# Kernel tuning notes

Hardware: AMD Instinct MI355X
Metric: run time of the kernel (lower is better)

The kernel has to match this reference:

```python
import jax, jax.numpy as jnp
import numpy as np

B, S, E, H = 4, 1024, 1024, 16
HD = E // H
MAX_SEQ = 5000


def setup_inputs() -> dict:
    key = jax.random.key(0)
    ks = jax.random.split(key, 10)
    def lin(kw, kb):
        w = jax.random.normal(kw, (E, E), dtype=jnp.float32) * (1.0 / np.sqrt(E))
        b = jax.random.normal(kb, (E,), dtype=jnp.float32) * 0.01
        return w, b
    wq, bq = lin(ks[0], ks[1])
    wk, bk = lin(ks[2], ks[3])
    wv, bv = lin(ks[4], ks[5])
    wo, bo = lin(ks[6], ks[7])
    rpe_table = jax.random.normal(ks[8], (H, 2 * MAX_SEQ - 1, HD), dtype=jnp.float32) * 0.02
    x = jax.random.normal(ks[9], (B, S, E), dtype=jnp.float32)
    return {"x": x, "wq": wq, "bq": bq, "wk": wk, "bk": bk,
            "wv": wv, "bv": bv, "wo": wo, "bo": bo, "rpe_table": rpe_table}


def reference(x, wq, bq, wk, bk, wv, bv, wo, bo, rpe_table):
    b, s, e = x.shape
    scale = 1.0 / np.sqrt(HD)
    # projections (torch Linear: y = x @ W^T + b), reshape to (b, h, s, hd)
    q = (x @ wq.T + bq).reshape(b, s, H, HD).transpose(0, 2, 1, 3)
    k = (x @ wk.T + bk).reshape(b, s, H, HD).transpose(0, 2, 1, 3)
    v = (x @ wv.T + bv).reshape(b, s, H, HD).transpose(0, 2, 1, 3)
    scores = jnp.einsum('bhqd,bhkd->bhqk', q, k) * scale
    # RPE: rpe[h, q, k, d] = table[h, q - k + s - 1, d]; factor the einsum:
    # rel[b,h,q,r] = sum_d q[b,h,q,d] * table[h,r,d], then gather r = q - k + s - 1
    table = rpe_table[:, : 2 * s - 1]               # (H, 2s-1, HD)
    rel = jnp.einsum('bhqd,hrd->bhqr', q, table)    # (b, H, s, 2s-1)
    idx = jnp.arange(s)[:, None] - jnp.arange(s)[None, :] + (s - 1)  # (s, s)
    rpe_scores = jnp.take_along_axis(
        rel, jnp.broadcast_to(idx[None, None], (b, H, s, s)), axis=-1)
    attn = jax.nn.softmax(scores + rpe_scores, axis=-1)
    ctx = jnp.einsum('bhqk,bhkd->bhqd', attn, v)
    ctx = ctx.transpose(0, 2, 1, 3).reshape(b, s, e)
    return ctx @ wo.T + bo
```

## Files before the change

kernel.cpp:

```cpp
#include <hip/hip_runtime.h>
#include <hip/hip_bf16.h>
#include <stdint.h>

typedef __attribute__((ext_vector_type(8))) short s8v;
typedef __attribute__((ext_vector_type(4))) float f32x4;
typedef __attribute__((ext_vector_type(16))) float f32x16;

union V16 { uint4 u4; unsigned int u[4]; s8v s; };

__device__ inline s8v u4_to_s8(uint4 v) { V16 c; c.u4 = v; return c.s; }
__device__ inline s8v words_to_s8(unsigned int a, unsigned int b, unsigned int c, unsigned int d) {
  V16 t; t.u[0] = a; t.u[1] = b; t.u[2] = c; t.u[3] = d; return t.s;
}
__device__ inline unsigned short f2b(float f) {
  __hip_bfloat16 h = __float2bfloat16(f);
  unsigned short u; __builtin_memcpy(&u, &h, 2); return u;
}
__device__ inline unsigned int pack2(float lo, float hi) {
  return ((unsigned int)f2b(hi) << 16) | (unsigned int)f2b(lo);
}
__device__ inline unsigned int cvtpk(float lo, float hi) {
  unsigned int r; asm("v_cvt_pk_bf16_f32 %0, %1, %2" : "=v"(r) : "v"(lo), "v"(hi)); return r;
}
__device__ inline float exp2_fast(float x) {
#if __has_builtin(__builtin_amdgcn_exp2f)
  return __builtin_amdgcn_exp2f(x);
#else
  float y; asm("v_exp_f32 %0, %1" : "=v"(y) : "v"(x)); return y;
#endif
}
__device__ inline void gld16(const void* g, void* lds) {
  __builtin_amdgcn_global_load_lds((const __attribute__((address_space(1))) void*)g,
                                   (__attribute__((address_space(3))) void*)lds, 16, 0, 0);
}

#define LOG2E 1.4426950408889634f

__global__ void cvt_fused_kernel(const float* __restrict__ x, const float* __restrict__ wq,
                                 const float* __restrict__ wk, const float* __restrict__ wv,
                                 const float* __restrict__ wo, const float* __restrict__ tb,
                                 __hip_bfloat16* __restrict__ XB, __hip_bfloat16* __restrict__ WQKV,
                                 __hip_bfloat16* __restrict__ WOb, __hip_bfloat16* __restrict__ TBL) {
  const int bid = blockIdx.x;
  if (bid < 4096) {
    size_t i = ((size_t)bid * 256 + threadIdx.x) * 8;
    const float* src; __hip_bfloat16* dst; size_t off;
    if (i < 4194304)      { src = x;  dst = XB;             off = i; }
    else if (i < 5242880) { src = wq; dst = WQKV;           off = i - 4194304; }
    else if (i < 6291456) { src = wk; dst = WQKV + 1048576; off = i - 5242880; }
    else if (i < 7340032) { src = wv; dst = WQKV + 2097152; off = i - 6291456; }
    else                  { src = wo; dst = WOb;            off = i - 7340032; }
    const float4* s4 = (const float4*)(src + off);
    float4 a = s4[0], b = s4[1];
    uint4 o;
    o.x = pack2(a.x, a.y); o.y = pack2(a.z, a.w);
    o.z = pack2(b.x, b.y); o.w = pack2(b.z, b.w);
    *(uint4*)(dst + off) = o;
  } else {
    size_t i = ((size_t)(bid - 4096) * 256 + threadIdx.x) * 8;
    int h = (int)(i >> 17);
    int rem = (int)(i & 131071);
    int r = rem >> 6, c = rem & 63;
    uint4 o;
    if (r < 2047) {
      const float4* s4 = (const float4*)(tb + ((size_t)h * 9999 + r) * 64 + c);
      float4 a = s4[0], b = s4[1];
      o.x = pack2(a.x * LOG2E, a.y * LOG2E); o.y = pack2(a.z * LOG2E, a.w * LOG2E);
      o.z = pack2(b.x * LOG2E, b.y * LOG2E); o.w = pack2(b.z * LOG2E, b.w * LOG2E);
    } else { o.x = 0u; o.y = 0u; o.z = 0u; o.w = 0u; }
    *(uint4*)(TBL + i) = o;
  }
}

__global__ __launch_bounds__(256, 3) void gemm_qkv(
    const __hip_bfloat16* __restrict__ A,
    const __hip_bfloat16* __restrict__ Bt,
    const float* __restrict__ bq, const float* __restrict__ bk, const float* __restrict__ bv,
    __hip_bfloat16* __restrict__ QB, __hip_bfloat16* __restrict__ KB,
    __hip_bfloat16* __restrict__ VTB) {
  __shared__ __align__(16) char smem[32768];
  char* As = smem;
  char* Bs = smem + 16384;
  const int tid = threadIdx.x;
  const int w = tid >> 6, l = tid & 63;
  const int wr = w >> 1, wc = w & 1;
  const int lr = l & 15, lg = l >> 4;
  const int m0 = blockIdx.y * 128, n0 = blockIdx.x * 128;

  f32x4 acc[4][4] = {};

  for (int kt = 0; kt < 16; ++kt) {
    __syncthreads();
    #pragma unroll
    for (int i = 0; i < 4; ++i) {
      const int off = i * 4096 + w * 1024;
      const int loff = off + l * 16;
      const int row = loff >> 7;
      const int cb = loff & 127;
      const int sc = cb ^ ((row & 7) << 4);
      gld16((const char*)A  + (size_t)(m0 + row) * 2048 + kt * 128 + sc, As + off);
      gld16((const char*)Bt + (size_t)(n0 + row) * 2048 + kt * 128 + sc, Bs + off);
    }
    asm volatile("s_waitcnt vmcnt(0)" ::: "memory");
    __syncthreads();
    #pragma unroll
    for (int ks = 0; ks < 2; ++ks) {
      uint4 af[4], bf4[4];
      #pragma unroll
      for (int i = 0; i < 4; ++i) {
        const int ra = wr * 64 + i * 16 + lr;
        const int rb = wc * 64 + i * 16 + lr;
        const int cb = ks * 64 + lg * 16;
        af[i]  = *(const uint4*)(As + ra * 128 + (cb ^ ((ra & 7) << 4)));
        bf4[i] = *(const uint4*)(Bs + rb * 128 + (cb ^ ((rb & 7) << 4)));
      }
      #pragma unroll
      for (int i = 0; i < 4; ++i) {
        #pragma unroll
        for (int j = 0; j < 4; ++j)
          acc[i][j] = __builtin_amdgcn_mfma_f32_16x16x32_bf16(u4_to_s8(af[i]), u4_to_s8(bf4[j]), acc[i][j], 0, 0, 0);
      }
    }
  }

  const int mrow = m0 + wr * 64 + lg * 4;
  const int ncol = n0 + wc * 64 + lr;
  const int cls = blockIdx.x >> 3;

  if (cls < 2) {
    const float sc = cls ? 0.125f * LOG2E : 1.0f;
    const float* bias = cls ? bk : bq;
    __hip_bfloat16* op = cls ? KB : QB;
    #pragma unroll
    for (int j = 0; j < 4; ++j) {
      const int n = ncol - cls * 1024 + j * 16;
      const float bia = bias[n];
      const int hh = n >> 6, hd = n & 63;
      #pragma unroll
      for (int i = 0; i < 4; ++i) {
        #pragma unroll
        for (int r = 0; r < 4; ++r) {
          const int m = mrow + i * 16 + r;
          const int bb = m >> 10, ss = m & 1023;
          op[(((size_t)(bb * 16 + hh)) * 1024 + ss) * 64 + hd] = __float2bfloat16((acc[i][j][r] + bia) * sc);
        }
      }
    }
  } else {
    #pragma unroll
    for (int j = 0; j < 4; ++j) {
      const int f = ncol - 2048 + j * 16;
      const float bia = bv[f];
      const int fh = f >> 6, fd = f & 63;
      #pragma unroll
      for (int i = 0; i < 4; ++i) {
        const int m = mrow + i * 16;
        const int bb = m >> 10, ss = m & 1023;
        ushort4 qv;
        qv.x = f2b(acc[i][j][0] + bia); qv.y = f2b(acc[i][j][1] + bia);
        qv.z = f2b(acc[i][j][2] + bia); qv.w = f2b(acc[i][j][3] + bia);
        *(ushort4*)((char*)VTB + (((size_t)bb * 1048576 + (size_t)fh * 65536 + fd * 1024 + ss) * 2)) = qv;
      }
    }
  }
}

__global__ __launch_bounds__(256, 3) void gemm_out(
    const __hip_bfloat16* __restrict__ A,
    const __hip_bfloat16* __restrict__ Bt,
    const float* __restrict__ bo,
    float* __restrict__ out) {
  __shared__ __align__(16) char smem[32768];
  char* As = smem;
  char* Bs = smem + 16384;
  const int tid = threadIdx.x;
  const int w = tid >> 6, l = tid & 63;
  const int wr = w >> 1, wc = w & 1;
  const int lr = l & 15, lg = l >> 4;
  const int m0 = blockIdx.y * 128, n0 = blockIdx.x * 128;

  f32x4 acc[4][4] = {};

  for (int kt = 0; kt < 16; ++kt) {
    __syncthreads();
    #pragma unroll
    for (int i = 0; i < 4; ++i) {
      const int off = i * 4096 + w * 1024;
      const int loff = off + l * 16;
      const int row = loff >> 7;
      const int cb = loff & 127;
      const int sc = cb ^ ((row & 7) << 4);
      gld16((const char*)A  + (size_t)(m0 + row) * 2048 + kt * 128 + sc, As + off);
      gld16((const char*)Bt + (size_t)(n0 + row) * 2048 + kt * 128 + sc, Bs + off);
    }
    asm volatile("s_waitcnt vmcnt(0)" ::: "memory");
    __syncthreads();
    #pragma unroll
    for (int ks = 0; ks < 2; ++ks) {
      uint4 af[4], bf4[4];
      #pragma unroll
      for (int i = 0; i < 4; ++i) {
        const int ra = wr * 64 + i * 16 + lr;
        const int rb = wc * 64 + i * 16 + lr;
        const int cb = ks * 64 + lg * 16;
        af[i]  = *(const uint4*)(As + ra * 128 + (cb ^ ((ra & 7) << 4)));
        bf4[i] = *(const uint4*)(Bs + rb * 128 + (cb ^ ((rb & 7) << 4)));
      }
      #pragma unroll
      for (int i = 0; i < 4; ++i) {
        #pragma unroll
        for (int j = 0; j < 4; ++j)
          acc[i][j] = __builtin_amdgcn_mfma_f32_16x16x32_bf16(u4_to_s8(af[i]), u4_to_s8(bf4[j]), acc[i][j], 0, 0, 0);
      }
    }
  }

  const int mrow = m0 + wr * 64 + lg * 4;
  const int ncol = n0 + wc * 64 + lr;
  #pragma unroll
  for (int j = 0; j < 4; ++j) {
    const int n = ncol + j * 16;
    const float bia = bo[n];
    #pragma unroll
    for (int i = 0; i < 4; ++i) {
      #pragma unroll
      for (int r = 0; r < 4; ++r) {
        const int m = mrow + i * 16 + r;
        out[(size_t)m * 1024 + n] = acc[i][j][r] + bia;
      }
    }
  }
}

__global__ __launch_bounds__(256, 2) void attn_kernel(
    const __hip_bfloat16* __restrict__ Qg,
    const __hip_bfloat16* __restrict__ Kg,
    const __hip_bfloat16* __restrict__ VTg,
    const __hip_bfloat16* __restrict__ Tg,
    __hip_bfloat16* __restrict__ Cg) {
  __shared__ __align__(16) char smem[73984];
  char* Klds = smem;
  char* Vlds = smem + 8192;
  char* Tlds = smem + 16384;
  const int tid = threadIdx.x;
  const int w = tid >> 6, l = tid & 63;
  const int ql = l & 31, half = l >> 5;
  char* relw = smem + 40960 + w * 8192;
  char* dumpp = smem + 73728 + l * 4;

  const int bx = blockIdx.x;
  const int work = (bx & 7) * 64 + (bx >> 3);
  const int b = work & 3, hqt = work >> 2;
  const int h = hqt >> 3, qt = hqt & 7;
  const int qb = qt * 128;
  const int q0 = qb + 32 * w;

  const size_t bh = (size_t)(b * 16 + h);
  const char* Qb = (const char*)Qg + bh * 131072;
  const char* Kb = (const char*)Kg + bh * 131072;
  const char* Vb = (const char*)VTg + bh * 131072;
  const char* Tb = (const char*)Tg + (size_t)h * 262144;

  const int relsw = ql * 256 + ((ql & 15) << 4);
  const int u4 = (ql << 2) - (half << 4);
  const int qlh = ql - 4 * half;
  const int k0sw = ql * 128 + ((ql & 7) << 4);
  const int k1sw = (32 + ql) * 128 + ((ql & 7) << 4);

  auto stageK = [&](int k0n) {
    #pragma unroll
    for (int i = 0; i < 2; ++i) {
      const int off = i * 4096 + w * 1024;
      const int loff = off + l * 16;
      const int row = loff >> 7, cb = loff & 127;
      const int sc = cb ^ ((row & 7) << 4);
      gld16(Kb + (size_t)(k0n + row) * 128 + sc, Klds + off);
    }
  };
  auto stageV = [&](int k0n) {
    #pragma unroll
    for (int i = 0; i < 2; ++i) {
      const int off = i * 4096 + w * 1024;
      const int loff = off + l * 16;
      const int row = loff >> 7, cb = loff & 127;
      const int sc = cb ^ ((row & 7) << 4);
      gld16(Vb + (size_t)row * 2048 + (size_t)k0n * 2 + sc, Vlds + off);
    }
  };
  auto stageT = [&](int rbn) {
    const int slot = (int)(((unsigned)(rbn >> 6)) % 3u);
    char* dst = Tlds + slot * 8192;
    #pragma unroll
    for (int i = 0; i < 2; ++i) {
      const int off = i * 4096 + w * 1024;
      const int loff = off + l * 16;
      const int row = loff >> 7, cb = loff & 127;
      const int sc = cb ^ ((row & 7) << 4);
      gld16(Tb + (size_t)(rbn + row) * 128 + sc, dst + off);
    }
  };

  s8v qv[4];
  {
    const char* qrow = Qb + (size_t)(q0 + ql) * 128 + half * 16;
    #pragma unroll
    for (int ds = 0; ds < 4; ++ds) qv[ds] = u4_to_s8(*(const uint4*)(qrow + ds * 32));
  }

  f32x16 cacc0 = {}, cacc1 = {};
  float mL = -1.0e30f, lsum = 0.0f;

  int rbase = qb + 960;

  stageK(0);
  stageT(rbase); stageT(rbase + 64); stageT(rbase + 128);
  stageV(0);

  for (int kt = 0; kt < 16; ++kt, rbase -= 64) {
    if (kt == 0) { asm volatile("s_waitcnt vmcnt(8)" ::: "memory"); }
    else         { asm volatile("s_waitcnt vmcnt(4)" ::: "memory"); }
    __builtin_amdgcn_s_barrier();

    f32x16 p0 = {}, p1 = {};
    __builtin_amdgcn_s_setprio(1);
    #pragma unroll
    for (int ds = 0; ds < 4; ++ds) {
      const int cb = ds * 32 + half * 16;
      uint4 kf0 = *(const uint4*)(Klds + (k0sw ^ cb));
      uint4 kf1 = *(const uint4*)(Klds + (k1sw ^ cb));
      p0 = __builtin_amdgcn_mfma_f32_32x32x16_bf16(u4_to_s8(kf0), qv[ds], p0, 0, 0, 0);
      p1 = __builtin_amdgcn_mfma_f32_32x32x16_bf16(u4_to_s8(kf1), qv[ds], p1, 0, 0, 0);
    }
    __builtin_amdgcn_s_setprio(0);

    __builtin_amdgcn_s_barrier();
    stageK(((kt + 1) & 15) * 64);

    asm volatile("s_waitcnt vmcnt(4)" ::: "memory");
    __builtin_amdgcn_s_barrier();

    __builtin_amdgcn_s_setprio(1);
    #pragma unroll
    for (int t = 0; t < 3; ++t) {
      const int slot = (int)(((unsigned)(rbase >> 6) + (unsigned)((w + t) >> 1)) % 3u);
      const int rowin = ((w + t) & 1) * 32 + ql;
      const int tbsw = slot * 8192 + rowin * 128 + ((ql & 7) << 4);
      f32x16 racc = {};
      #pragma unroll
      for (int ds = 0; ds < 4; ++ds) {
        const int cb = ds * 32 + half * 16;
        uint4 tf = *(const uint4*)(Tlds + (tbsw ^ cb));
        racc = __builtin_amdgcn_mfma_f32_32x32x16_bf16(u4_to_s8(tf), qv[ds], racc, 0, 0, 0);
      }
      #pragma unroll
      for (int g = 0; g < 4; ++g) {
        #pragma unroll
        for (int j = 0; j < 4; ++j) {
          const int C4 = 4 * (63 - 32 * t - j - 8 * g);
          char* dst = relw + (relsw ^ ((u4 + C4) & 252));
          if (t == 2) dst = (j + 8 * g < qlh) ? dst : dumpp;
          *(float*)dst = racc[4 * g + j];
        }
      }
    }
    __builtin_amdgcn_s_setprio(0);

    __builtin_amdgcn_s_barrier();
    { int rbn = rbase - 64; if (rbn < 0) rbn = 0; stageT(rbn); }

    #pragma unroll
    for (int mp = 0; mp < 4; ++mp) {
      const int X0 = 32 * mp + 16 * half;
      f32x4 r0 = *(const f32x4*)(relw + (relsw ^ X0));
      f32x4 r1 = *(const f32x4*)(relw + (relsw ^ (X0 + 128)));
      #pragma unroll
      for (int j = 0; j < 4; ++j) {
        p0[4 * mp + j] += r0[j];
        p1[4 * mp + j] += r1[j];
      }
    }

    float mx[8];
    #pragma unroll
    for (int i = 0; i < 8; ++i)
      mx[i] = fmaxf(fmaxf(p0[2 * i], p0[2 * i + 1]), fmaxf(p1[2 * i], p1[2 * i + 1]));
    float pmax = fmaxf(fmaxf(fmaxf(mx[0], mx[1]), fmaxf(mx[2], mx[3])),
                       fmaxf(fmaxf(mx[4], mx[5]), fmaxf(mx[6], mx[7])));
    pmax = fmaxf(pmax, __shfl_xor(pmax, 32));
    if (!__all(pmax - mL <= 12.0f)) {
      const float mnew = fmaxf(mL, pmax);
      const float corr = exp2_fast(mL - mnew);
      mL = mnew;
      lsum *= corr;
      #pragma unroll
      for (int r = 0; r < 16; ++r) {
        const float cr = __shfl(corr, (r & 3) + 8 * (r >> 2) + 4 * half);
        cacc0[r] *= cr;
        cacc1[r] *= cr;
      }
    }
    #pragma unroll
    for (int r = 0; r < 16; ++r) {
      p0[r] = exp2_fast(p0[r] - mL);
      p1[r] = exp2_fast(p1[r] - mL);
    }
    float sm[8];
    #pragma unroll
    for (int i = 0; i < 8; ++i)
      sm[i] = (p0[2 * i] + p0[2 * i + 1]) + (p1[2 * i] + p1[2 * i + 1]);
    float psum = ((sm[0] + sm[1]) + (sm[2] + sm[3])) + ((sm[4] + sm[5]) + (sm[6] + sm[7]));
    psum += __shfl_xor(psum, 32);
    lsum += psum;

    unsigned int w0[8], w1[8];
    #pragma unroll
    for (int jw = 0; jw < 8; ++jw) {
      w0[jw] = cvtpk(p0[2 * jw], p0[2 * jw + 1]);
      w1[jw] = cvtpk(p1[2 * jw], p1[2 * jw + 1]);
    }
    unsigned int r0x[4], r1x[4];
    #pragma unroll
    for (int i = 0; i < 4; ++i) {
      const int jkeep = (i & 1) + 4 * (i >> 1);
      const int jsend = jkeep + 2;
      unsigned int v0 = half ? w0[jkeep] : w0[jsend];
      unsigned int v1 = half ? w1[jkeep] : w1[jsend];
      r0x[i] = (unsigned int)__shfl_xor((int)v0, 32);
      r1x[i] = (unsigned int)__shfl_xor((int)v1, 32);
    }

    asm volatile("s_waitcnt vmcnt(4)" ::: "memory");
    __builtin_amdgcn_s_barrier();

    __builtin_amdgcn_s_setprio(1);
    #pragma unroll
    for (int ks = 0; ks < 4; ++ks) {
      const int mm = ks & 1;
      unsigned int f0_, f1_, f2_, f3_;
      if (ks < 2) {
        f0_ = half ? r0x[2 * mm]     : w0[4 * mm];
        f1_ = half ? r0x[2 * mm + 1] : w0[4 * mm + 1];
        f2_ = half ? w0[4 * mm + 2]  : r0x[2 * mm];
        f3_ = half ? w0[4 * mm + 3]  : r0x[2 * mm + 1];
      } else {
        f0_ = half ? r1x[2 * mm]     : w1[4 * mm];
        f1_ = half ? r1x[2 * mm + 1] : w1[4 * mm + 1];
        f2_ = half ? w1[4 * mm + 2]  : r1x[2 * mm];
        f3_ = half ? w1[4 * mm + 3]  : r1x[2 * mm + 1];
      }
      s8v pf = words_to_s8(f0_, f1_, f2_, f3_);
      const int cb = ks * 32 + half * 16;
      uint4 vf0 = *(const uint4*)(Vlds + (k0sw ^ cb));
      uint4 vf1 = *(const uint4*)(Vlds + (k1sw ^ cb));
      cacc0 = __builtin_amdgcn_mfma_f32_32x32x16_bf16(pf, u4_to_s8(vf0), cacc0, 0, 0, 0);
      cacc1 = __builtin_amdgcn_mfma_f32_32x32x16_bf16(pf, u4_to_s8(vf1), cacc1, 0, 0, 0);
    }
    __builtin_amdgcn_s_setprio(0);

    __builtin_amdgcn_s_barrier();
    stageV(((kt + 1) & 15) * 64);
  }
  asm volatile("s_waitcnt vmcnt(0)" ::: "memory");

  #pragma unroll
  for (int r = 0; r < 16; ++r) {
    const int qr = (r & 3) + 8 * (r >> 2) + 4 * half;
    const float inv = 1.0f / __shfl(lsum, qr);
    const size_t row = (size_t)b * 1024 + q0 + qr;
    const size_t basei = row * 1024 + h * 64 + ql;
    Cg[basei]      = __float2bfloat16(cacc0[r] * inv);
    Cg[basei + 32] = __float2bfloat16(cacc1[r] * inv);
  }
}

extern "C" void kernel_launch(void* const* d_in, const int* in_sizes, int n_in,
                              void* d_out, int out_size, void* d_ws, size_t ws_size,
                              hipStream_t stream) {
  (void)in_sizes; (void)n_in; (void)out_size; (void)ws_size;
  const float* x  = (const float*)d_in[0];
  const float* wq = (const float*)d_in[1];
  const float* bq = (const float*)d_in[2];
  const float* wk = (const float*)d_in[3];
  const float* bk = (const float*)d_in[4];
  const float* wv = (const float*)d_in[5];
  const float* bv = (const float*)d_in[6];
  const float* wo = (const float*)d_in[7];
  const float* bo = (const float*)d_in[8];
  const float* tb = (const float*)d_in[9];

  char* ws = (char*)d_ws;
  __hip_bfloat16* XB   = (__hip_bfloat16*)(ws);
  __hip_bfloat16* WQKV = (__hip_bfloat16*)(ws + 8388608);
  __hip_bfloat16* WOb  = (__hip_bfloat16*)(ws + 14680064);
  __hip_bfloat16* TBL  = (__hip_bfloat16*)(ws + 16777216);
  __hip_bfloat16* QB   = (__hip_bfloat16*)(ws + 20971520);
  __hip_bfloat16* KB   = (__hip_bfloat16*)(ws + 29360128);
  __hip_bfloat16* VTB  = (__hip_bfloat16*)(ws + 37748736);
  __hip_bfloat16* CTX  = (__hip_bfloat16*)(ws + 46137344);

  cvt_fused_kernel<<<5120, 256, 0, stream>>>(x, wq, wk, wv, wo, tb, XB, WQKV, WOb, TBL);
  gemm_qkv<<<dim3(24, 32), 256, 0, stream>>>(XB, WQKV, bq, bk, bv, QB, KB, VTB);
  attn_kernel<<<512, 256, 0, stream>>>(QB, KB, VTB, TBL, CTX);
  gemm_out<<<dim3(8, 32), 256, 0, stream>>>(CTX, WOb, bo, (float*)d_out);
}
```

Baseline: 113.9 us.

## Load V fragments directly to registers, double-buffer K, and cut attention barriers

V tiles are no longer staged through LDS. Each lane loads its own V fragments from global memory into registers for the next key tile, prefetched during the current iteration. K becomes double-buffered, the RPE table ring grows from three to four slots, and the relative-score scatter is rewritten to drop the dump slot, so the loop needs one barrier per iteration instead of four. The goal is less barrier stall and LDS traffic, at the cost of more VGPRs (8 uint4 held per lane), more LDS, and tighter vmcnt accounting that could be fragile.

```diff
diff --git a/kernel.cpp b/kernel.cpp
--- a/kernel.cpp
+++ b/kernel.cpp
@@ -238,15 +238,13 @@
     const __hip_bfloat16* __restrict__ VTg,
     const __hip_bfloat16* __restrict__ Tg,
     __hip_bfloat16* __restrict__ Cg) {
-  __shared__ __align__(16) char smem[73984];
+  __shared__ __align__(16) char smem[81920];
   char* Klds = smem;
-  char* Vlds = smem + 8192;
   char* Tlds = smem + 16384;
   const int tid = threadIdx.x;
   const int w = tid >> 6, l = tid & 63;
   const int ql = l & 31, half = l >> 5;
-  char* relw = smem + 40960 + w * 8192;
-  char* dumpp = smem + 73728 + l * 4;
+  char* relw = smem + 49152 + w * 8192;
 
   const int bx = blockIdx.x;
   const int work = (bx & 7) * 64 + (bx >> 3);
@@ -263,40 +261,26 @@
 
   const int relsw = ql * 256 + ((ql & 15) << 4);
   const int u4 = (ql << 2) - (half << 4);
-  const int qlh = ql - 4 * half;
   const int k0sw = ql * 128 + ((ql & 7) << 4);
   const int k1sw = (32 + ql) * 128 + ((ql & 7) << 4);
 
-  auto stageK = [&](int k0n) {
+  auto stageK = [&](int k0n, int buf) {
     #pragma unroll
     for (int i = 0; i < 2; ++i) {
-      const int off = i * 4096 + w * 1024;
-      const int loff = off + l * 16;
+      const int loff = i * 4096 + w * 1024 + l * 16;
       const int row = loff >> 7, cb = loff & 127;
       const int sc = cb ^ ((row & 7) << 4);
-      gld16(Kb + (size_t)(k0n + row) * 128 + sc, Klds + off);
+      gld16(Kb + (size_t)(k0n + row) * 128 + sc, Klds + buf * 8192 + i * 4096 + w * 1024);
     }
   };
-  auto stageV = [&](int k0n) {
+  auto stageT = [&](int rsrc, int slot) {
+    char* dst = Tlds + slot * 8192;
     #pragma unroll
     for (int i = 0; i < 2; ++i) {
-      const int off = i * 4096 + w * 1024;
-      const int loff = off + l * 16;
+      const int loff = i * 4096 + w * 1024 + l * 16;
       const int row = loff >> 7, cb = loff & 127;
       const int sc = cb ^ ((row & 7) << 4);
-      gld16(Vb + (size_t)row * 2048 + (size_t)k0n * 2 + sc, Vlds + off);
-    }
-  };
-  auto stageT = [&](int rbn) {
-    const int slot = (int)(((unsigned)(rbn >> 6)) % 3u);
-    char* dst = Tlds + slot * 8192;
-    #pragma unroll
-    for (int i = 0; i < 2; ++i) {
-      const int off = i * 4096 + w * 1024;
-      const int loff = off + l * 16;
-      const int row = loff >> 7, cb = loff & 127;
-      const int sc = cb ^ ((row & 7) << 4);
-      gld16(Tb + (size_t)(rbn + row) * 128 + sc, dst + off);
+      gld16(Tb + (size_t)(rsrc + row) * 128 + sc, dst + i * 4096 + w * 1024);
     }
   };
 
@@ -309,64 +293,67 @@
 
   f32x16 cacc0 = {}, cacc1 = {};
   float mL = -1.0e30f, lsum = 0.0f;
-
   int rbase = qb + 960;
 
-  stageK(0);
-  stageT(rbase); stageT(rbase + 64); stageT(rbase + 128);
-  stageV(0);
+  stageK(0, 0);
+  stageT(rbase,       ((rbase >> 6) + 0) & 3);
+  stageT(rbase + 64,  ((rbase >> 6) + 1) & 3);
+  stageT(rbase + 128, ((rbase >> 6) + 2) & 3);
+  __builtin_amdgcn_sched_barrier(0);
+  uint4 vr[8];
+  #pragma unroll
+  for (int t = 0; t < 2; ++t)
+    #pragma unroll
+    for (int ks = 0; ks < 4; ++ks)
+      vr[t * 4 + ks] = *(const uint4*)(Vb + (size_t)(t * 32 + ql) * 2048 + ks * 32 + half * 16);
+  asm volatile("s_waitcnt vmcnt(8)" ::: "memory");
+  __builtin_amdgcn_s_barrier();
 
   for (int kt = 0; kt < 16; ++kt, rbase -= 64) {
-    if (kt == 0) { asm volatile("s_waitcnt vmcnt(8)" ::: "memory"); }
-    else         { asm volatile("s_waitcnt vmcnt(4)" ::: "memory"); }
-    __builtin_amdgcn_s_barrier();
-
+    stageK(((kt + 1) & 15) * 64, (kt + 1) & 1);
+    { const int rbn = rbase - 64;
+      stageT(rbn < 0 ? 0 : rbn, (rbn >> 6) & 3); }
+
+    const int kb = (kt & 1) * 8192;
     f32x16 p0 = {}, p1 = {};
     __builtin_amdgcn_s_setprio(1);
     #pragma unroll
     for (int ds = 0; ds < 4; ++ds) {
       const int cb = ds * 32 + half * 16;
-      uint4 kf0 = *(const uint4*)(Klds + (k0sw ^ cb));
-      uint4 kf1 = *(const uint4*)(Klds + (k1sw ^ cb));
+      uint4 kf0 = *(const uint4*)(Klds + kb + (k0sw ^ cb));
+      uint4 kf1 = *(const uint4*)(Klds + kb + (k1sw ^ cb));
       p0 = __builtin_amdgcn_mfma_f32_32x32x16_bf16(u4_to_s8(kf0), qv[ds], p0, 0, 0, 0);
       p1 = __builtin_amdgcn_mfma_f32_32x32x16_bf16(u4_to_s8(kf1), qv[ds], p1, 0, 0, 0);
     }
     __builtin_amdgcn_s_setprio(0);
 
-    __builtin_amdgcn_s_barrier();
-    stageK(((kt + 1) & 15) * 64);
-
-    asm volatile("s_waitcnt vmcnt(4)" ::: "memory");
-    __builtin_amdgcn_s_barrier();
-
-    __builtin_amdgcn_s_setprio(1);
-    #pragma unroll
-    for (int t = 0; t < 3; ++t) {
-      const int slot = (int)(((unsigned)(rbase >> 6) + (unsigned)((w + t) >> 1)) % 3u);
-      const int rowin = ((w + t) & 1) * 32 + ql;
+    #pragma unroll
+    for (int ti = 0; ti < 3; ++ti) {
+      const int bt = (ti == 0) ? 2 : ((ti == 1) ? 0 : 1);
+      const int slot = ((rbase >> 6) + ((w + bt) >> 1)) & 3;
+      const int rowin = ((w + bt) & 1) * 32 + ql;
       const int tbsw = slot * 8192 + rowin * 128 + ((ql & 7) << 4);
       f32x16 racc = {};
+      __builtin_amdgcn_s_setprio(1);
       #pragma unroll
       for (int ds = 0; ds < 4; ++ds) {
         const int cb = ds * 32 + half * 16;
         uint4 tf = *(const uint4*)(Tlds + (tbsw ^ cb));
         racc = __builtin_amdgcn_mfma_f32_32x32x16_bf16(u4_to_s8(tf), qv[ds], racc, 0, 0, 0);
       }
+      __builtin_amdgcn_s_setprio(0);
       #pragma unroll
       for (int g = 0; g < 4; ++g) {
         #pragma unroll
         for (int j = 0; j < 4; ++j) {
-          const int C4 = 4 * (63 - 32 * t - j - 8 * g);
-          char* dst = relw + (relsw ^ ((u4 + C4) & 252));
-          if (t == 2) dst = (j + 8 * g < qlh) ? dst : dumpp;
-          *(float*)dst = racc[4 * g + j];
+          int pos4;
+          if (bt == 2)      pos4 = (u4 + 4 * (-1 - j - 8 * g)) & 124;
+          else if (bt == 0) pos4 = ((u4 + 4 * (63 - j - 8 * g)) & 252) | 128;
+          else              pos4 = (u4 + 4 * (31 - j - 8 * g)) & 252;
+          *(float*)(relw + (relsw ^ pos4)) = racc[4 * g + j];
         }
       }
     }
-    __builtin_amdgcn_s_setprio(0);
-
-    __builtin_amdgcn_s_barrier();
-    { int rbn = rbase - 64; if (rbn < 0) rbn = 0; stageT(rbn); }
 
     #pragma unroll
     for (int mp = 0; mp < 4; ++mp) {
@@ -430,7 +417,6 @@
     }
 
     asm volatile("s_waitcnt vmcnt(4)" ::: "memory");
-    __builtin_amdgcn_s_barrier();
 
     __builtin_amdgcn_s_setprio(1);
     #pragma unroll
@@ -449,16 +435,21 @@
         f3_ = half ? w1[4 * mm + 3]  : r1x[2 * mm + 1];
       }
       s8v pf = words_to_s8(f0_, f1_, f2_, f3_);
-      const int cb = ks * 32 + half * 16;
-      uint4 vf0 = *(const uint4*)(Vlds + (k0sw ^ cb));
-      uint4 vf1 = *(const uint4*)(Vlds + (k1sw ^ cb));
-      cacc0 = __builtin_amdgcn_mfma_f32_32x32x16_bf16(pf, u4_to_s8(vf0), cacc0, 0, 0, 0);
-      cacc1 = __builtin_amdgcn_mfma_f32_32x32x16_bf16(pf, u4_to_s8(vf1), cacc1, 0, 0, 0);
+      cacc0 = __builtin_amdgcn_mfma_f32_32x32x16_bf16(pf, u4_to_s8(vr[ks]), cacc0, 0, 0, 0);
+      cacc1 = __builtin_amdgcn_mfma_f32_32x32x16_bf16(pf, u4_to_s8(vr[4 + ks]), cacc1, 0, 0, 0);
     }
     __builtin_amdgcn_s_setprio(0);
 
+    { const int kn2 = ((kt + 1) & 15) * 128;
+      #pragma unroll
+      for (int t = 0; t < 2; ++t)
+        #pragma unroll
+        for (int ks = 0; ks < 4; ++ks)
+          vr[t * 4 + ks] = *(const uint4*)(Vb + (size_t)(t * 32 + ql) * 2048 + kn2 + ks * 32 + half * 16);
+    }
+
+    asm volatile("s_waitcnt vmcnt(8)" ::: "memory");
     __builtin_amdgcn_s_barrier();
-    stageV(((kt + 1) & 15) * 64);
   }
   asm volatile("s_waitcnt vmcnt(0)" ::: "memory");
 
```

Result: no change. 114.7 us (+0.7%).
